# Kernel optimization log

Hardware: AMD Instinct MI355X
Metric: run time of the kernel (lower is better)

The kernel has to match this reference:

```python
import jax, jax.numpy as jnp
import numpy as np

DIM = 512
DIM_TIME = 64
DIM_FF = 2048
B, L = 2, 512
EPS = 1e-5


def _layer_norm(x, g, b):
    mu = jnp.mean(x, axis=-1, keepdims=True)
    var = jnp.mean((x - mu) ** 2, axis=-1, keepdims=True)
    return (x - mu) * jax.lax.rsqrt(var + EPS) * g + b


def _sioconv(u, wa, hid_re, hid_im):
    # u: (B, L, Dt) float. Faithful to the FFT/triu construction, expressed as
    # cumulative log-sums (linear conv with all-ones == causal cumsum).
    Bb, Ll, Dt = u.shape
    out = (u @ wa.T).reshape(Bb, Ll, Dt, 2)          # linear_a, view_as_complex
    a_sqr = out[..., 0] ** 2 + out[..., 1] ** 2
    a = (out[..., 0] + 1j * out[..., 1]) * (jax.lax.rsqrt(a_sqr) * jnp.exp(-a_sqr))
    a = jnp.transpose(a, (0, 2, 1))                  # (B, Dt, L)
    a_ln = jnp.log(a)
    S = jnp.cumsum(a_ln, axis=-1)                    # S_k = sum_{j<=k} ln a_j
    S_prev = jnp.concatenate([jnp.zeros_like(S[..., :1]), S[..., :-1]], axis=-1)
    # c[b,d,i,k] = exp(S_k - S_{i-1}) = prod_{j=i..k} a_j, kept for k >= i-1
    diff = S[:, :, None, :] - S_prev[:, :, :, None]  # (B, Dt, L, L)
    idx = jnp.arange(Ll)
    mask = idx[None, :] >= (idx[:, None] - 1)        # k >= i-1 (triu diag=-1)
    c = jnp.where(mask, jnp.exp(diff), 0.0)
    uc = jnp.transpose(u.astype(jnp.complex64), (0, 2, 1))   # (B, Dt, L)
    hidden = (hid_re + 1j * hid_im)[None, :] * jnp.ones((Bb, 1), jnp.complex64)
    xin = jnp.concatenate([hidden[..., None], uc[..., :-1]], axis=-1)  # rolled + h0
    h = jnp.einsum('bdik,bdk->bdi', c, xin)
    h = h.at[:, :, -1].add(uc[:, :, -1])
    return jnp.transpose(h.real, (0, 2, 1)).astype(u.dtype)


def _ffn(x, w1, b1, w2, b2):
    return jax.nn.silu(x @ w1.T + b1) @ w2.T + b2


def setup_inputs() -> dict:
    key = jax.random.key(0)
    ks = jax.random.split(key, 12)
    d, dt, dff = DIM, DIM_TIME, DIM_FF
    return {
        'x': jax.random.normal(ks[0], (B, L, d), jnp.float32),
        'ln1_g': jnp.ones((d,), jnp.float32), 'ln1_b': jnp.zeros((d,), jnp.float32),
        'fc_w': jax.random.normal(ks[1], (dt, d), jnp.float32) * d ** -0.5,
        'fc_b': jnp.zeros((dt,), jnp.float32),
        'lin_in_w': jax.random.normal(ks[2], (dt, d), jnp.float32) * d ** -0.5,
        'lin_in_b': jnp.zeros((dt,), jnp.float32),
        'wa': jax.random.normal(ks[3], (2 * dt, dt), jnp.float32) * dt ** -0.5,
        'hid_re': jax.random.normal(ks[4], (dt,), jnp.float32),
        'hid_im': jax.random.normal(ks[5], (dt,), jnp.float32),
        'lin_out_w': jax.random.normal(ks[6], (d, dt), jnp.float32) * dt ** -0.5,
        'lin_out_b': jnp.zeros((d,), jnp.float32),
        'ln2_g': jnp.ones((d,), jnp.float32), 'ln2_b': jnp.zeros((d,), jnp.float32),
        'w1': jax.random.normal(ks[7], (dff, d), jnp.float32) * d ** -0.5,
        'b1': jnp.zeros((dff,), jnp.float32),
        'w2': jax.random.normal(ks[8], (d, dff), jnp.float32) * dff ** -0.5,
        'b2': jnp.zeros((d,), jnp.float32),
    }


def reference(x, ln1_g, ln1_b, fc_w, fc_b, lin_in_w, lin_in_b, wa, hid_re, hid_im,
              lin_out_w, lin_out_b, ln2_g, ln2_b, w1, b1, w2, b2):
    x_res = x
    xn = _layer_norm(x, ln1_g, ln1_b)
    y = jax.nn.silu(xn @ fc_w.T + fc_b)                  # gate, (B, L, Dt)
    u = xn @ lin_in_w.T + lin_in_b                       # (B, L, Dt)
    h = _sioconv(u, wa, hid_re, hid_im)
    x = (h * y) @ lin_out_w.T + lin_out_b + x_res        # dropout = identity (eval)
    x_res = x
    x = _ffn(_layer_norm(x, ln2_g, ln2_b), w1, b1, w2, b2) + x_res
    return x
```

## Files before the change

### kernel.cpp

```cpp
#include <hip/hip_runtime.h>
#include <math.h>

#define LSEQ 512
#define DMODEL 512
#define DT 64
#define DFF 2048

typedef unsigned short u16;
typedef __attribute__((ext_vector_type(8))) short short8;
typedef __attribute__((ext_vector_type(4))) float f32x4;

__device__ __forceinline__ float wave_sum(float v) {
#pragma unroll
  for (int o = 32; o > 0; o >>= 1) v += __shfl_xor(v, o, 64);
  return v;
}

__device__ __forceinline__ u16 f2bf(float f) {
  unsigned int u = __float_as_uint(f);
  u += 0x7fffu + ((u >> 16) & 1u);
  return (u16)(u >> 16);
}
__device__ __forceinline__ float bf2f(u16 h) {
  return __uint_as_float(((unsigned int)h) << 16);
}
__device__ __forceinline__ void splitbf(float f, u16& h, u16& l) {
  h = f2bf(f);
  l = f2bf(f - bf2f(h));
}

__device__ __forceinline__ void gload_lds16(const void* g, void* l) {
  __builtin_amdgcn_global_load_lds(
      (const __attribute__((address_space(1))) unsigned int*)g,
      (__attribute__((address_space(3))) unsigned int*)l, 16, 0, 0);
}

__global__ __launch_bounds__(256) void k_cvtall(
    const float* __restrict__ w1, const float* __restrict__ w2,
    const float* __restrict__ fcw, const float* __restrict__ liw,
    const float* __restrict__ wa, const float* __restrict__ low,
    u16* __restrict__ w1b, u16* __restrict__ w2b,
    u16* __restrict__ fclh, u16* __restrict__ fcll,
    u16* __restrict__ wah, u16* __restrict__ wal,
    u16* __restrict__ lowh, u16* __restrict__ lowl)
{
  int i = blockIdx.x * 256 + threadIdx.x;
  if (i >= 550912) return;
  if (i < 524288) {
    const float* s = (i < 262144) ? w1 : w2;
    u16* d = (i < 262144) ? w1b : w2b;
    int off = (i < 262144) ? i : i - 262144;
    float4 v = ((const float4*)s)[off];
    ushort4 o;
    o.x = f2bf(v.x); o.y = f2bf(v.y); o.z = f2bf(v.z); o.w = f2bf(v.w);
    ((ushort4*)d)[off] = o;
    return;
  }
  const float* s; int j; u16 *dh, *dl;
  if (i < 532480)      { s = fcw; j = i - 524288;        dh = fclh; dl = fcll; }
  else if (i < 540672) { s = liw; j = i - 532480 + 8192; dh = fclh; dl = fcll; }
  else if (i < 542720) { s = wa;  j = i - 540672;        dh = wah;  dl = wal;  }
  else                 { s = low; j = i - 542720;        dh = lowh; dl = lowl; }
  int soff = (i < 532480) ? i - 524288 :
             (i < 540672) ? i - 532480 :
             (i < 542720) ? i - 540672 : i - 542720;
  float4 v = ((const float4*)s)[soff];
  ushort4 oh, ol;
  splitbf(v.x, oh.x, ol.x); splitbf(v.y, oh.y, ol.y);
  splitbf(v.z, oh.z, ol.z); splitbf(v.w, oh.w, ol.w);
  ((ushort4*)dh)[j] = oh;
  ((ushort4*)dl)[j] = ol;
}

template<int LO>
__global__ __launch_bounds__(256) void k_ln(
    const float* __restrict__ in, const float* __restrict__ g,
    const float* __restrict__ be, u16* __restrict__ outh, u16* __restrict__ outl)
{
  const int lane = threadIdx.x & 63, wv = threadIdx.x >> 6;
  const int row = blockIdx.x * 4 + wv;
  const float* xr = in + (size_t)row * DMODEL;
  float v[8]; float s = 0.f;
#pragma unroll
  for (int j = 0; j < 8; ++j) { v[j] = xr[lane + 64 * j]; s += v[j]; }
  s = wave_sum(s);
  const float mu = s * (1.f / 512.f);
  float q = 0.f;
#pragma unroll
  for (int j = 0; j < 8; ++j) { float dd = v[j] - mu; q += dd * dd; }
  q = wave_sum(q);
  const float rstd = rsqrtf(q * (1.f / 512.f) + 1e-5f);
#pragma unroll
  for (int j = 0; j < 8; ++j) {
    int idx = lane + 64 * j;
    float o = (v[j] - mu) * rstd * g[idx] + be[idx];
    if constexpr (LO) {
      u16 h, l; splitbf(o, h, l);
      outh[(size_t)row * DMODEL + idx] = h;
      outl[(size_t)row * DMODEL + idx] = l;
    } else {
      outh[(size_t)row * DMODEL + idx] = f2bf(o);
    }
  }
}

__global__ __launch_bounds__(256) void k_proj(
    const u16* __restrict__ xnh, const u16* __restrict__ xnl,
    const u16* __restrict__ fclh, const u16* __restrict__ fcll,
    const float* __restrict__ fcb, const float* __restrict__ lib,
    float* __restrict__ y_o, float* __restrict__ u_o,
    u16* __restrict__ ubh, u16* __restrict__ ubl)
{
  const int w = threadIdx.x >> 6, lane = threadIdx.x & 63;
  const int mt = blockIdx.x, nt = blockIdx.y * 4 + w;
  const int lr = lane & 15, lk = lane >> 4;
  const size_t aoff = (size_t)(mt * 16 + lr) * DMODEL + lk * 8;
  const size_t boff = (size_t)(nt * 16 + lr) * DMODEL + lk * 8;
  f32x4 acc = {};
#pragma unroll 4
  for (int k = 0; k < DMODEL; k += 32) {
    short8 ah = *(const short8*)(xnh + aoff + k);
    short8 al = *(const short8*)(xnl + aoff + k);
    short8 bh = *(const short8*)(fclh + boff + k);
    short8 bl = *(const short8*)(fcll + boff + k);
    acc = __builtin_amdgcn_mfma_f32_16x16x32_bf16(ah, bh, acc, 0, 0, 0);
    acc = __builtin_amdgcn_mfma_f32_16x16x32_bf16(ah, bl, acc, 0, 0, 0);
    acc = __builtin_amdgcn_mfma_f32_16x16x32_bf16(al, bh, acc, 0, 0, 0);
  }
  const int c = nt * 16 + lr;
#pragma unroll
  for (int j = 0; j < 4; ++j) {
    int row = mt * 16 + lk * 4 + j;
    float v = acc[j];
    if (c < DT) {
      v += fcb[c];
      y_o[row * DT + c] = v / (1.f + expf(-v));
    } else {
      int d = c - DT;
      v += lib[d];
      u_o[row * DT + d] = v;
      u16 h, l; splitbf(v, h, l);
      ubh[row * DT + d] = h;
      ubl[row * DT + d] = l;
    }
  }
}

__global__ __launch_bounds__(256) void k_au(
    const u16* __restrict__ ubh, const u16* __restrict__ ubl,
    const u16* __restrict__ wah, const u16* __restrict__ wal,
    float* __restrict__ ar_o, float* __restrict__ ai_o)
{
  const int w = threadIdx.x >> 6, lane = threadIdx.x & 63;
  const int mt = blockIdx.x, nt = blockIdx.y * 4 + w;
  const int lr = lane & 15, lk = lane >> 4;
  const size_t aoff = (size_t)(mt * 16 + lr) * DT + lk * 8;
  const size_t boff = (size_t)(nt * 16 + lr) * DT + lk * 8;
  f32x4 acc = {};
#pragma unroll
  for (int k = 0; k < DT; k += 32) {
    short8 ah = *(const short8*)(ubh + aoff + k);
    short8 al = *(const short8*)(ubl + aoff + k);
    short8 bh = *(const short8*)(wah + boff + k);
    short8 bl = *(const short8*)(wal + boff + k);
    acc = __builtin_amdgcn_mfma_f32_16x16x32_bf16(ah, bh, acc, 0, 0, 0);
    acc = __builtin_amdgcn_mfma_f32_16x16x32_bf16(ah, bl, acc, 0, 0, 0);
    acc = __builtin_amdgcn_mfma_f32_16x16x32_bf16(al, bh, acc, 0, 0, 0);
  }
  const int c = nt * 16 + lr;
#pragma unroll
  for (int j = 0; j < 4; ++j) {
    float v = acc[j];
    float p = __shfl_xor(v, 1, 64);
    float re = (lane & 1) ? p : v;
    float im = (lane & 1) ? v : p;
    float asq = re * re + im * im;
    float sc = rsqrtf(asq) * expf(-asq);
    int row = mt * 16 + lk * 4 + j;
    int d = c >> 1;
    if (lane & 1) ai_o[row * DT + d] = im * sc;
    else          ar_o[row * DT + d] = re * sc;
  }
}

__global__ __launch_bounds__(64) void k_scan2(
    const float* __restrict__ u, const float* __restrict__ ar, const float* __restrict__ ai,
    const float* __restrict__ hr, const float* __restrict__ hi, float* __restrict__ h_o)
{
  const int blk = blockIdx.x;
  const int b = blk >> 6, d = blk & 63;
  const int lane = threadIdx.x;
  const size_t base = (size_t)b * LSEQ * DT + d;
  const int i0 = lane * 8;

  float a_r[8], a_i[8], b_r[8], b_i[8];
#pragma unroll
  for (int e = 0; e < 8; ++e) {
    int i = i0 + e;
    a_r[e] = ar[base + (size_t)i * DT];
    a_i[e] = ai[base + (size_t)i * DT];
    if (i >= 2)      { b_r[e] = u[base + (size_t)(i - 2) * DT]; b_i[e] = 0.f; }
    else if (i == 1) { b_r[e] = hr[d]; b_i[e] = hi[d]; }
    else             { b_r[e] = 0.f;   b_i[e] = 0.f; }
  }

  float Ar = 1.f, Ai = 0.f, Br = 0.f, Bi = 0.f;
#pragma unroll
  for (int e = 0; e < 8; ++e) {
    float nBr = fmaf(Ar, b_r[e], fmaf(-Ai, b_i[e], Br));
    float nBi = fmaf(Ar, b_i[e], fmaf( Ai, b_r[e], Bi));
    float nAr = Ar * a_r[e] - Ai * a_i[e];
    float nAi = Ar * a_i[e] + Ai * a_r[e];
    Ar = nAr; Ai = nAi; Br = nBr; Bi = nBi;
  }

#pragma unroll
  for (int dlt = 1; dlt < 64; dlt <<= 1) {
    float Ar2 = __shfl_down(Ar, dlt, 64);
    float Ai2 = __shfl_down(Ai, dlt, 64);
    float Br2 = __shfl_down(Br, dlt, 64);
    float Bi2 = __shfl_down(Bi, dlt, 64);
    if (lane + dlt < 64) {
      float nAr = Ar * Ar2 - Ai * Ai2;
      float nAi = Ar * Ai2 + Ai * Ar2;
      float nBr = fmaf(Ar, Br2, fmaf(-Ai, Bi2, Br));
      float nBi = fmaf(Ar, Bi2, fmaf( Ai, Br2, Bi));
      Ar = nAr; Ai = nAi; Br = nBr; Bi = nBi;
    }
  }

  float A1r = __shfl_down(Ar, 1, 64), A1i = __shfl_down(Ai, 1, 64);
  float B1r = __shfl_down(Br, 1, 64), B1i = __shfl_down(Bi, 1, 64);
  if (lane == 63) { A1r = 1.f; A1i = 0.f; B1r = 0.f; B1i = 0.f; }
  const float r512 = u[base + (size_t)(LSEQ - 2) * DT];
  float rr = fmaf(A1r, r512, B1r);
  float ri = fmaf(A1i, r512, B1i);

  const float uL = u[base + (size_t)(LSEQ - 1) * DT];
#pragma unroll
  for (int e = 7; e >= 0; --e) {
    int i = i0 + e;
    float nr = fmaf(a_r[e], rr, fmaf(-a_i[e], ri, b_r[e]));
    float ni = fmaf(a_r[e], ri, fmaf( a_i[e], rr, b_i[e]));
    rr = nr; ri = ni;
    float outv = rr;
    if (i == LSEQ - 1) outv += uL;
    h_o[base + (size_t)i * DT] = outv;
  }
}

__global__ __launch_bounds__(256) void k_mid2(
    const float* __restrict__ h, const float* __restrict__ y,
    const u16* __restrict__ lowh, const u16* __restrict__ lowl,
    const float* __restrict__ lob, const float* __restrict__ x,
    float* __restrict__ x2_o)
{
  const int w = threadIdx.x >> 6, lane = threadIdx.x & 63;
  const int mt = blockIdx.x, nt = blockIdx.y * 4 + w;
  const int lr = lane & 15, lk = lane >> 4;
  const int arow = mt * 16 + lr;
  const float* hp = h + (size_t)arow * DT + lk * 8;
  const float* yp = y + (size_t)arow * DT + lk * 8;
  const size_t boff = (size_t)(nt * 16 + lr) * DT + lk * 8;
  f32x4 acc = {};
#pragma unroll
  for (int ks = 0; ks < 2; ++ks) {
    float4 h0 = *(const float4*)(hp + ks * 32);
    float4 h1 = *(const float4*)(hp + ks * 32 + 4);
    float4 y0 = *(const float4*)(yp + ks * 32);
    float4 y1 = *(const float4*)(yp + ks * 32 + 4);
    float pv[8] = {h0.x * y0.x, h0.y * y0.y, h0.z * y0.z, h0.w * y0.w,
                   h1.x * y1.x, h1.y * y1.y, h1.z * y1.z, h1.w * y1.w};
    short8 ah, al;
#pragma unroll
    for (int e = 0; e < 8; ++e) {
      u16 hh, ll; splitbf(pv[e], hh, ll);
      ah[e] = (short)hh; al[e] = (short)ll;
    }
    short8 bh = *(const short8*)(lowh + boff + ks * 32);
    short8 bl = *(const short8*)(lowl + boff + ks * 32);
    acc = __builtin_amdgcn_mfma_f32_16x16x32_bf16(ah, bh, acc, 0, 0, 0);
    acc = __builtin_amdgcn_mfma_f32_16x16x32_bf16(ah, bl, acc, 0, 0, 0);
    acc = __builtin_amdgcn_mfma_f32_16x16x32_bf16(al, bh, acc, 0, 0, 0);
  }
  const int c = nt * 16 + lr;
#pragma unroll
  for (int j = 0; j < 4; ++j) {
    int row = mt * 16 + lk * 4 + j;
    x2_o[(size_t)row * DMODEL + c] = acc[j] + lob[c] + x[(size_t)row * DMODEL + c];
  }
}

template<int BM, int BN, int EPI>
__global__ __launch_bounds__(256) void k_mfma(
    const u16* __restrict__ A, const u16* __restrict__ B,
    const float* __restrict__ bias, float* __restrict__ Cf, u16* __restrict__ Cb,
    int K, int N, int kTiles, int partStride)
{
  constexpr int MF = BM / 32, NF = BN / 32;
  __shared__ __align__(16) u16 As[BM * 64];
  __shared__ __align__(16) u16 Bs[BN * 64];
  const int t = threadIdx.x;
  const int m0 = blockIdx.x * BM, n0 = blockIdx.y * BN;
  const int kBase = blockIdx.z * kTiles * 64;
  const int w = t >> 6, lane = t & 63;
  const int wm = w >> 1, wn = w & 1;
  const int lr = lane & 15, lk = lane >> 4;
  f32x4 acc[MF][NF] = {};

  for (int kt = 0; kt < kTiles; ++kt) {
    const int k0 = kBase + kt * 64;
#pragma unroll
    for (int i = 0; i < BM / 32; ++i) {
      int e = i * 2048 + t * 8;
      int row = e >> 6, col = e & 63;
      gload_lds16(A + (size_t)(m0 + row) * K + k0 + col, &As[e]);
    }
#pragma unroll
    for (int i = 0; i < BN / 32; ++i) {
      int e = i * 2048 + t * 8;
      int row = e >> 6, col = e & 63;
      gload_lds16(B + (size_t)(n0 + row) * K + k0 + col, &Bs[e]);
    }
    __syncthreads();
#pragma unroll
    for (int ks = 0; ks < 2; ++ks) {
      short8 af[MF], bf[NF];
#pragma unroll
      for (int mf = 0; mf < MF; ++mf)
        af[mf] = *(const short8*)&As[(wm * (BM / 2) + mf * 16 + lr) * 64 + ks * 32 + lk * 8];
#pragma unroll
      for (int nf = 0; nf < NF; ++nf)
        bf[nf] = *(const short8*)&Bs[(wn * (BN / 2) + nf * 16 + lr) * 64 + ks * 32 + lk * 8];
#pragma unroll
      for (int mf = 0; mf < MF; ++mf)
#pragma unroll
        for (int nf = 0; nf < NF; ++nf)
          acc[mf][nf] = __builtin_amdgcn_mfma_f32_16x16x32_bf16(af[mf], bf[nf], acc[mf][nf], 0, 0, 0);
    }
    __syncthreads();
  }

#pragma unroll
  for (int mf = 0; mf < MF; ++mf)
#pragma unroll
    for (int nf = 0; nf < NF; ++nf)
#pragma unroll
      for (int j = 0; j < 4; ++j) {
        int rrow = m0 + wm * (BM / 2) + mf * 16 + lk * 4 + j;
        int ccol = n0 + wn * (BN / 2) + nf * 16 + lr;
        if constexpr (EPI == 0) {
          float v = acc[mf][nf][j] + bias[ccol];
          v = v / (1.f + expf(-v));
          Cb[(size_t)rrow * N + ccol] = f2bf(v);
        } else {
          Cf[(size_t)blockIdx.z * partStride + (size_t)rrow * N + ccol] = acc[mf][nf][j];
        }
      }
}

__global__ __launch_bounds__(256) void k_red(
    const float* __restrict__ p, const float* __restrict__ b2,
    const float* __restrict__ x2, float* __restrict__ out, int n4, int partStride4)
{
  int i = blockIdx.x * 256 + threadIdx.x;
  if (i >= n4) return;
  const float4* p4 = (const float4*)p;
  float4 s = p4[i];
  float4 s1 = p4[i + partStride4];
  float4 s2 = p4[i + 2 * partStride4];
  float4 s3 = p4[i + 3 * partStride4];
  s.x += s1.x; s.y += s1.y; s.z += s1.z; s.w += s1.w;
  s.x += s2.x; s.y += s2.y; s.z += s2.z; s.w += s2.w;
  s.x += s3.x; s.y += s3.y; s.z += s3.z; s.w += s3.w;
  int col4 = i & 127;
  float4 bb = ((const float4*)b2)[col4];
  float4 rr = ((const float4*)x2)[i];
  s.x += bb.x + rr.x; s.y += bb.y + rr.y; s.z += bb.z + rr.z; s.w += bb.w + rr.w;
  ((float4*)out)[i] = s;
}

extern "C" void kernel_launch(void* const* d_in, const int* in_sizes, int n_in,
                              void* d_out, int out_size, void* d_ws, size_t ws_size,
                              hipStream_t stream) {
  const float* x    = (const float*)d_in[0];
  const float* ln1g = (const float*)d_in[1];
  const float* ln1b = (const float*)d_in[2];
  const float* fcw  = (const float*)d_in[3];
  const float* fcb  = (const float*)d_in[4];
  const float* liw  = (const float*)d_in[5];
  const float* lib  = (const float*)d_in[6];
  const float* wa   = (const float*)d_in[7];
  const float* hidr = (const float*)d_in[8];
  const float* hidi = (const float*)d_in[9];
  const float* low  = (const float*)d_in[10];
  const float* lob  = (const float*)d_in[11];
  const float* ln2g = (const float*)d_in[12];
  const float* ln2b = (const float*)d_in[13];
  const float* w1   = (const float*)d_in[14];
  const float* b1   = (const float*)d_in[15];
  const float* w2   = (const float*)d_in[16];
  const float* b2   = (const float*)d_in[17];
  float* out = (float*)d_out;
  float* ws  = (float*)d_ws;

  const int R = 2 * LSEQ;
  float* y_    = ws;
  float* u_    = y_   + 65536;
  float* ar_   = u_   + 65536;
  float* ai_   = ar_  + 65536;
  float* h_    = ai_  + 65536;
  float* x2_   = h_   + 65536;
  float* part_ = x2_  + 524288;
  u16* p = (u16*)(part_ + 2097152);
  u16* xnh  = p;            p += 524288;
  u16* xnl  = p;            p += 524288;
  u16* xn2b = p;            p += 524288;
  u16* ubh  = p;            p += 65536;
  u16* ubl  = p;            p += 65536;
  u16* h1b  = p;            p += 2097152;
  u16* w1b  = p;            p += 1048576;
  u16* w2b  = p;            p += 1048576;
  u16* fclh = p;            p += 65536;
  u16* fcll = p;            p += 65536;
  u16* wah  = p;            p += 8192;
  u16* wal  = p;            p += 8192;
  u16* lowh = p;            p += 32768;
  u16* lowl = p;            p += 32768;

  k_cvtall<<<2152, 256, 0, stream>>>(w1, w2, fcw, liw, wa, low,
                                     w1b, w2b, fclh, fcll, wah, wal, lowh, lowl);
  k_ln<1><<<256, 256, 0, stream>>>(x, ln1g, ln1b, xnh, xnl);
  k_proj<<<dim3(64, 2), 256, 0, stream>>>(xnh, xnl, fclh, fcll, fcb, lib,
                                          y_, u_, ubh, ubl);
  k_au<<<dim3(64, 2), 256, 0, stream>>>(ubh, ubl, wah, wal, ar_, ai_);
  k_scan2<<<128, 64, 0, stream>>>(u_, ar_, ai_, hidr, hidi, h_);
  k_mid2<<<dim3(64, 8), 256, 0, stream>>>(h_, y_, lowh, lowl, lob, x, x2_);
  k_ln<0><<<256, 256, 0, stream>>>(x2_, ln2g, ln2b, xn2b, nullptr);
  dim3 g1(R / 64, DFF / 64);
  k_mfma<64, 64, 0><<<g1, 256, 0, stream>>>(xn2b, w1b, b1, nullptr, h1b,
                                            DMODEL, DFF, DMODEL / 64, 0);
  dim3 g2(R / 64, DMODEL / 64, 4);
  k_mfma<64, 64, 2><<<g2, 256, 0, stream>>>(h1b, w2b, nullptr, part_, nullptr,
                                            DFF, DMODEL, (DFF / 4) / 64, R * DMODEL);
  k_red<<<(R * DMODEL / 4 + 255) / 256, 256, 0, stream>>>(part_, b2, x2_, out,
                                                          R * DMODEL / 4, R * DMODEL / 4);
}
```

Baseline: 62.47 us.

## Fuse kernels across pipeline and rewrite FFN GEMMs with 32x32 MFMA

Merges LN1 into the weight-conversion kernel, fuses the projection and linear_a GEMMs into one kernel with the intermediate kept in LDS, and fuses lin_out with LN2. It also replaces the LDS-tiled FFN GEMMs with direct-from-global 32x32x16 MFMA kernels, using an in-block split-K reduction that drops the separate partial-sum reduce kernel. Launch count falls from 10 to 6 and global round trips shrink, but the new FFN kernels read operands without LDS reuse and the fused kernels run with fewer blocks (64).

```diff
diff --git a/kernel.cpp b/kernel.cpp
--- a/kernel.cpp
+++ b/kernel.cpp
@@ -9,6 +9,7 @@
 typedef unsigned short u16;
 typedef __attribute__((ext_vector_type(8))) short short8;
 typedef __attribute__((ext_vector_type(4))) float f32x4;
+typedef __attribute__((ext_vector_type(16))) float f32x16;
 
 __device__ __forceinline__ float wave_sum(float v) {
 #pragma unroll
@@ -29,21 +30,42 @@
   l = f2bf(f - bf2f(h));
 }
 
-__device__ __forceinline__ void gload_lds16(const void* g, void* l) {
-  __builtin_amdgcn_global_load_lds(
-      (const __attribute__((address_space(1))) unsigned int*)g,
-      (__attribute__((address_space(3))) unsigned int*)l, 16, 0, 0);
-}
-
-__global__ __launch_bounds__(256) void k_cvtall(
+__global__ __launch_bounds__(256) void k_pre(
     const float* __restrict__ w1, const float* __restrict__ w2,
     const float* __restrict__ fcw, const float* __restrict__ liw,
     const float* __restrict__ wa, const float* __restrict__ low,
+    const float* __restrict__ x, const float* __restrict__ g1,
+    const float* __restrict__ be1,
     u16* __restrict__ w1b, u16* __restrict__ w2b,
     u16* __restrict__ fclh, u16* __restrict__ fcll,
     u16* __restrict__ wah, u16* __restrict__ wal,
-    u16* __restrict__ lowh, u16* __restrict__ lowl)
-{
+    u16* __restrict__ lowh, u16* __restrict__ lowl,
+    u16* __restrict__ xnh, u16* __restrict__ xnl)
+{
+  if (blockIdx.x >= 2152) {
+    const int lane = threadIdx.x & 63, wv = threadIdx.x >> 6;
+    const int row = (blockIdx.x - 2152) * 4 + wv;
+    const float* xr = x + (size_t)row * DMODEL;
+    float v[8]; float s = 0.f;
+#pragma unroll
+    for (int j = 0; j < 8; ++j) { v[j] = xr[lane + 64 * j]; s += v[j]; }
+    s = wave_sum(s);
+    const float mu = s * (1.f / 512.f);
+    float q = 0.f;
+#pragma unroll
+    for (int j = 0; j < 8; ++j) { float dd = v[j] - mu; q += dd * dd; }
+    q = wave_sum(q);
+    const float rstd = rsqrtf(q * (1.f / 512.f) + 1e-5f);
+#pragma unroll
+    for (int j = 0; j < 8; ++j) {
+      int idx = lane + 64 * j;
+      float o = (v[j] - mu) * rstd * g1[idx] + be1[idx];
+      u16 h, l; splitbf(o, h, l);
+      xnh[(size_t)row * DMODEL + idx] = h;
+      xnl[(size_t)row * DMODEL + idx] = l;
+    }
+    return;
+  }
   int i = blockIdx.x * 256 + threadIdx.x;
   if (i >= 550912) return;
   if (i < 524288) {
@@ -72,114 +94,80 @@
   ((ushort4*)dl)[j] = ol;
 }
 
-template<int LO>
-__global__ __launch_bounds__(256) void k_ln(
-    const float* __restrict__ in, const float* __restrict__ g,
-    const float* __restrict__ be, u16* __restrict__ outh, u16* __restrict__ outl)
-{
-  const int lane = threadIdx.x & 63, wv = threadIdx.x >> 6;
-  const int row = blockIdx.x * 4 + wv;
-  const float* xr = in + (size_t)row * DMODEL;
-  float v[8]; float s = 0.f;
-#pragma unroll
-  for (int j = 0; j < 8; ++j) { v[j] = xr[lane + 64 * j]; s += v[j]; }
-  s = wave_sum(s);
-  const float mu = s * (1.f / 512.f);
-  float q = 0.f;
-#pragma unroll
-  for (int j = 0; j < 8; ++j) { float dd = v[j] - mu; q += dd * dd; }
-  q = wave_sum(q);
-  const float rstd = rsqrtf(q * (1.f / 512.f) + 1e-5f);
-#pragma unroll
-  for (int j = 0; j < 8; ++j) {
-    int idx = lane + 64 * j;
-    float o = (v[j] - mu) * rstd * g[idx] + be[idx];
-    if constexpr (LO) {
-      u16 h, l; splitbf(o, h, l);
-      outh[(size_t)row * DMODEL + idx] = h;
-      outl[(size_t)row * DMODEL + idx] = l;
-    } else {
-      outh[(size_t)row * DMODEL + idx] = f2bf(o);
-    }
-  }
-}
-
-__global__ __launch_bounds__(256) void k_proj(
+__global__ __launch_bounds__(512) void k_fa(
     const u16* __restrict__ xnh, const u16* __restrict__ xnl,
     const u16* __restrict__ fclh, const u16* __restrict__ fcll,
+    const u16* __restrict__ wah, const u16* __restrict__ wal,
     const float* __restrict__ fcb, const float* __restrict__ lib,
     float* __restrict__ y_o, float* __restrict__ u_o,
-    u16* __restrict__ ubh, u16* __restrict__ ubl)
-{
+    float* __restrict__ ar_o, float* __restrict__ ai_o)
+{
+  __shared__ __align__(16) u16 ush[16][80];
+  __shared__ __align__(16) u16 usl[16][80];
   const int w = threadIdx.x >> 6, lane = threadIdx.x & 63;
-  const int mt = blockIdx.x, nt = blockIdx.y * 4 + w;
+  const int mt = blockIdx.x;
   const int lr = lane & 15, lk = lane >> 4;
-  const size_t aoff = (size_t)(mt * 16 + lr) * DMODEL + lk * 8;
-  const size_t boff = (size_t)(nt * 16 + lr) * DMODEL + lk * 8;
-  f32x4 acc = {};
+
+  {
+    const size_t aoff = (size_t)(mt * 16 + lr) * DMODEL + lk * 8;
+    const size_t boff = (size_t)(w * 16 + lr) * DMODEL + lk * 8;
+    f32x4 acc = {};
 #pragma unroll 4
-  for (int k = 0; k < DMODEL; k += 32) {
-    short8 ah = *(const short8*)(xnh + aoff + k);
-    short8 al = *(const short8*)(xnl + aoff + k);
-    short8 bh = *(const short8*)(fclh + boff + k);
-    short8 bl = *(const short8*)(fcll + boff + k);
-    acc = __builtin_amdgcn_mfma_f32_16x16x32_bf16(ah, bh, acc, 0, 0, 0);
-    acc = __builtin_amdgcn_mfma_f32_16x16x32_bf16(ah, bl, acc, 0, 0, 0);
-    acc = __builtin_amdgcn_mfma_f32_16x16x32_bf16(al, bh, acc, 0, 0, 0);
-  }
-  const int c = nt * 16 + lr;
-#pragma unroll
-  for (int j = 0; j < 4; ++j) {
-    int row = mt * 16 + lk * 4 + j;
-    float v = acc[j];
-    if (c < DT) {
-      v += fcb[c];
-      y_o[row * DT + c] = v / (1.f + expf(-v));
-    } else {
-      int d = c - DT;
-      v += lib[d];
-      u_o[row * DT + d] = v;
-      u16 h, l; splitbf(v, h, l);
-      ubh[row * DT + d] = h;
-      ubl[row * DT + d] = l;
-    }
-  }
-}
-
-__global__ __launch_bounds__(256) void k_au(
-    const u16* __restrict__ ubh, const u16* __restrict__ ubl,
-    const u16* __restrict__ wah, const u16* __restrict__ wal,
-    float* __restrict__ ar_o, float* __restrict__ ai_o)
-{
-  const int w = threadIdx.x >> 6, lane = threadIdx.x & 63;
-  const int mt = blockIdx.x, nt = blockIdx.y * 4 + w;
-  const int lr = lane & 15, lk = lane >> 4;
-  const size_t aoff = (size_t)(mt * 16 + lr) * DT + lk * 8;
-  const size_t boff = (size_t)(nt * 16 + lr) * DT + lk * 8;
-  f32x4 acc = {};
-#pragma unroll
-  for (int k = 0; k < DT; k += 32) {
-    short8 ah = *(const short8*)(ubh + aoff + k);
-    short8 al = *(const short8*)(ubl + aoff + k);
-    short8 bh = *(const short8*)(wah + boff + k);
-    short8 bl = *(const short8*)(wal + boff + k);
-    acc = __builtin_amdgcn_mfma_f32_16x16x32_bf16(ah, bh, acc, 0, 0, 0);
-    acc = __builtin_amdgcn_mfma_f32_16x16x32_bf16(ah, bl, acc, 0, 0, 0);
-    acc = __builtin_amdgcn_mfma_f32_16x16x32_bf16(al, bh, acc, 0, 0, 0);
-  }
-  const int c = nt * 16 + lr;
-#pragma unroll
-  for (int j = 0; j < 4; ++j) {
-    float v = acc[j];
-    float p = __shfl_xor(v, 1, 64);
-    float re = (lane & 1) ? p : v;
-    float im = (lane & 1) ? v : p;
-    float asq = re * re + im * im;
-    float sc = rsqrtf(asq) * expf(-asq);
-    int row = mt * 16 + lk * 4 + j;
-    int d = c >> 1;
-    if (lane & 1) ai_o[row * DT + d] = im * sc;
-    else          ar_o[row * DT + d] = re * sc;
+    for (int k = 0; k < DMODEL; k += 32) {
+      short8 ah = *(const short8*)(xnh + aoff + k);
+      short8 al = *(const short8*)(xnl + aoff + k);
+      short8 bh = *(const short8*)(fclh + boff + k);
+      short8 bl = *(const short8*)(fcll + boff + k);
+      acc = __builtin_amdgcn_mfma_f32_16x16x32_bf16(ah, bh, acc, 0, 0, 0);
+      acc = __builtin_amdgcn_mfma_f32_16x16x32_bf16(ah, bl, acc, 0, 0, 0);
+      acc = __builtin_amdgcn_mfma_f32_16x16x32_bf16(al, bh, acc, 0, 0, 0);
+    }
+    const int c = w * 16 + lr;
+#pragma unroll
+    for (int j = 0; j < 4; ++j) {
+      int rl = lk * 4 + j;
+      int row = mt * 16 + rl;
+      float v = acc[j];
+      if (c < DT) {
+        v += fcb[c];
+        y_o[row * DT + c] = v / (1.f + expf(-v));
+      } else {
+        int d = c - DT;
+        v += lib[d];
+        u_o[row * DT + d] = v;
+        u16 h, l; splitbf(v, h, l);
+        ush[rl][d] = h; usl[rl][d] = l;
+      }
+    }
+  }
+  __syncthreads();
+  {
+    const size_t boff = (size_t)(w * 16 + lr) * DT + lk * 8;
+    f32x4 acc = {};
+#pragma unroll
+    for (int ks = 0; ks < 2; ++ks) {
+      short8 ah = *(const short8*)&ush[lr][ks * 32 + lk * 8];
+      short8 al = *(const short8*)&usl[lr][ks * 32 + lk * 8];
+      short8 bh = *(const short8*)(wah + boff + ks * 32);
+      short8 bl = *(const short8*)(wal + boff + ks * 32);
+      acc = __builtin_amdgcn_mfma_f32_16x16x32_bf16(ah, bh, acc, 0, 0, 0);
+      acc = __builtin_amdgcn_mfma_f32_16x16x32_bf16(ah, bl, acc, 0, 0, 0);
+      acc = __builtin_amdgcn_mfma_f32_16x16x32_bf16(al, bh, acc, 0, 0, 0);
+    }
+    const int c = w * 16 + lr;
+#pragma unroll
+    for (int j = 0; j < 4; ++j) {
+      float v = acc[j];
+      float p = __shfl_xor(v, 1, 64);
+      float re = (lane & 1) ? p : v;
+      float im = (lane & 1) ? v : p;
+      float asq = re * re + im * im;
+      float sc = rsqrtf(asq) * expf(-asq);
+      int row = mt * 16 + lk * 4 + j;
+      int d = c >> 1;
+      if (lane & 1) ai_o[row * DT + d] = im * sc;
+      else          ar_o[row * DT + d] = re * sc;
+    }
   }
 }
 
@@ -249,135 +237,131 @@
   }
 }
 
-__global__ __launch_bounds__(256) void k_mid2(
+__global__ __launch_bounds__(512) void k_midln(
     const float* __restrict__ h, const float* __restrict__ y,
     const u16* __restrict__ lowh, const u16* __restrict__ lowl,
     const float* __restrict__ lob, const float* __restrict__ x,
-    float* __restrict__ x2_o)
+    const float* __restrict__ g2, const float* __restrict__ be2,
+    float* __restrict__ x2_o, u16* __restrict__ xn2b)
+{
+  __shared__ __align__(16) u16 hyh[16][80];
+  __shared__ __align__(16) u16 hyl[16][80];
+  __shared__ float x2s[16][520];
+  const int tid = threadIdx.x;
+  const int w = tid >> 6, lane = tid & 63;
+  const int lr = lane & 15, lk = lane >> 4;
+  const int mt = blockIdx.x;
+
+  for (int s = tid; s < 16 * DT; s += 512) {
+    int r = s >> 6, d = s & 63;
+    int row = mt * 16 + r;
+    float v = h[row * DT + d] * y[row * DT + d];
+    u16 hh, ll; splitbf(v, hh, ll);
+    hyh[r][d] = hh; hyl[r][d] = ll;
+  }
+  __syncthreads();
+
+#pragma unroll
+  for (int t = 0; t < 4; ++t) {
+    const int nt = w * 4 + t;
+    const size_t boff = (size_t)(nt * 16 + lr) * DT + lk * 8;
+    f32x4 acc = {};
+#pragma unroll
+    for (int ks = 0; ks < 2; ++ks) {
+      short8 ah = *(const short8*)&hyh[lr][ks * 32 + lk * 8];
+      short8 al = *(const short8*)&hyl[lr][ks * 32 + lk * 8];
+      short8 bh = *(const short8*)(lowh + boff + ks * 32);
+      short8 bl = *(const short8*)(lowl + boff + ks * 32);
+      acc = __builtin_amdgcn_mfma_f32_16x16x32_bf16(ah, bh, acc, 0, 0, 0);
+      acc = __builtin_amdgcn_mfma_f32_16x16x32_bf16(ah, bl, acc, 0, 0, 0);
+      acc = __builtin_amdgcn_mfma_f32_16x16x32_bf16(al, bh, acc, 0, 0, 0);
+    }
+    const int c = nt * 16 + lr;
+#pragma unroll
+    for (int j = 0; j < 4; ++j) {
+      int rl = lk * 4 + j;
+      int row = mt * 16 + rl;
+      float v = acc[j] + lob[c] + x[(size_t)row * DMODEL + c];
+      x2s[rl][c] = v;
+      x2_o[(size_t)row * DMODEL + c] = v;
+    }
+  }
+  __syncthreads();
+
+#pragma unroll
+  for (int rr = 0; rr < 2; ++rr) {
+    const int r = w * 2 + rr;
+    const int row = mt * 16 + r;
+    float v[8]; float s = 0.f;
+#pragma unroll
+    for (int j = 0; j < 8; ++j) { v[j] = x2s[r][lane + 64 * j]; s += v[j]; }
+    s = wave_sum(s);
+    const float mu = s * (1.f / 512.f);
+    float q = 0.f;
+#pragma unroll
+    for (int j = 0; j < 8; ++j) { float dd = v[j] - mu; q += dd * dd; }
+    q = wave_sum(q);
+    const float rstd = rsqrtf(q * (1.f / 512.f) + 1e-5f);
+#pragma unroll
+    for (int j = 0; j < 8; ++j) {
+      int idx = lane + 64 * j;
+      xn2b[(size_t)row * DMODEL + idx] = f2bf((v[j] - mu) * rstd * g2[idx] + be2[idx]);
+    }
+  }
+}
+
+__global__ __launch_bounds__(256) void k_ffn1(
+    const u16* __restrict__ A, const u16* __restrict__ B,
+    const float* __restrict__ bias, u16* __restrict__ C)
 {
   const int w = threadIdx.x >> 6, lane = threadIdx.x & 63;
   const int mt = blockIdx.x, nt = blockIdx.y * 4 + w;
-  const int lr = lane & 15, lk = lane >> 4;
-  const int arow = mt * 16 + lr;
-  const float* hp = h + (size_t)arow * DT + lk * 8;
-  const float* yp = y + (size_t)arow * DT + lk * 8;
-  const size_t boff = (size_t)(nt * 16 + lr) * DT + lk * 8;
-  f32x4 acc = {};
-#pragma unroll
-  for (int ks = 0; ks < 2; ++ks) {
-    float4 h0 = *(const float4*)(hp + ks * 32);
-    float4 h1 = *(const float4*)(hp + ks * 32 + 4);
-    float4 y0 = *(const float4*)(yp + ks * 32);
-    float4 y1 = *(const float4*)(yp + ks * 32 + 4);
-    float pv[8] = {h0.x * y0.x, h0.y * y0.y, h0.z * y0.z, h0.w * y0.w,
-                   h1.x * y1.x, h1.y * y1.y, h1.z * y1.z, h1.w * y1.w};
-    short8 ah, al;
-#pragma unroll
-    for (int e = 0; e < 8; ++e) {
-      u16 hh, ll; splitbf(pv[e], hh, ll);
-      ah[e] = (short)hh; al[e] = (short)ll;
-    }
-    short8 bh = *(const short8*)(lowh + boff + ks * 32);
-    short8 bl = *(const short8*)(lowl + boff + ks * 32);
-    acc = __builtin_amdgcn_mfma_f32_16x16x32_bf16(ah, bh, acc, 0, 0, 0);
-    acc = __builtin_amdgcn_mfma_f32_16x16x32_bf16(ah, bl, acc, 0, 0, 0);
-    acc = __builtin_amdgcn_mfma_f32_16x16x32_bf16(al, bh, acc, 0, 0, 0);
-  }
-  const int c = nt * 16 + lr;
-#pragma unroll
-  for (int j = 0; j < 4; ++j) {
-    int row = mt * 16 + lk * 4 + j;
-    x2_o[(size_t)row * DMODEL + c] = acc[j] + lob[c] + x[(size_t)row * DMODEL + c];
-  }
-}
-
-template<int BM, int BN, int EPI>
-__global__ __launch_bounds__(256) void k_mfma(
+  const int l32 = lane & 31, hi = lane >> 5;
+  const u16* a = A + (size_t)(mt * 32 + l32) * DMODEL + hi * 8;
+  const u16* b = B + (size_t)(nt * 32 + l32) * DMODEL + hi * 8;
+  f32x16 acc = {};
+#pragma unroll 8
+  for (int k = 0; k < DMODEL; k += 16)
+    acc = __builtin_amdgcn_mfma_f32_32x32x16_bf16(*(const short8*)(a + k),
+                                                  *(const short8*)(b + k), acc, 0, 0, 0);
+  const int col = nt * 32 + l32;
+  const float bb = bias[col];
+#pragma unroll
+  for (int r = 0; r < 16; ++r) {
+    int row = mt * 32 + (r & 3) + 8 * (r >> 2) + 4 * hi;
+    float v = acc[r] + bb;
+    v = v / (1.f + expf(-v));
+    C[(size_t)row * DFF + col] = f2bf(v);
+  }
+}
+
+__global__ __launch_bounds__(256) void k_ffn2(
     const u16* __restrict__ A, const u16* __restrict__ B,
-    const float* __restrict__ bias, float* __restrict__ Cf, u16* __restrict__ Cb,
-    int K, int N, int kTiles, int partStride)
-{
-  constexpr int MF = BM / 32, NF = BN / 32;
-  __shared__ __align__(16) u16 As[BM * 64];
-  __shared__ __align__(16) u16 Bs[BN * 64];
-  const int t = threadIdx.x;
-  const int m0 = blockIdx.x * BM, n0 = blockIdx.y * BN;
-  const int kBase = blockIdx.z * kTiles * 64;
-  const int w = t >> 6, lane = t & 63;
-  const int wm = w >> 1, wn = w & 1;
-  const int lr = lane & 15, lk = lane >> 4;
-  f32x4 acc[MF][NF] = {};
-
-  for (int kt = 0; kt < kTiles; ++kt) {
-    const int k0 = kBase + kt * 64;
-#pragma unroll
-    for (int i = 0; i < BM / 32; ++i) {
-      int e = i * 2048 + t * 8;
-      int row = e >> 6, col = e & 63;
-      gload_lds16(A + (size_t)(m0 + row) * K + k0 + col, &As[e]);
-    }
-#pragma unroll
-    for (int i = 0; i < BN / 32; ++i) {
-      int e = i * 2048 + t * 8;
-      int row = e >> 6, col = e & 63;
-      gload_lds16(B + (size_t)(n0 + row) * K + k0 + col, &Bs[e]);
-    }
-    __syncthreads();
-#pragma unroll
-    for (int ks = 0; ks < 2; ++ks) {
-      short8 af[MF], bf[NF];
-#pragma unroll
-      for (int mf = 0; mf < MF; ++mf)
-        af[mf] = *(const short8*)&As[(wm * (BM / 2) + mf * 16 + lr) * 64 + ks * 32 + lk * 8];
-#pragma unroll
-      for (int nf = 0; nf < NF; ++nf)
-        bf[nf] = *(const short8*)&Bs[(wn * (BN / 2) + nf * 16 + lr) * 64 + ks * 32 + lk * 8];
-#pragma unroll
-      for (int mf = 0; mf < MF; ++mf)
-#pragma unroll
-        for (int nf = 0; nf < NF; ++nf)
-          acc[mf][nf] = __builtin_amdgcn_mfma_f32_16x16x32_bf16(af[mf], bf[nf], acc[mf][nf], 0, 0, 0);
-    }
-    __syncthreads();
-  }
-
-#pragma unroll
-  for (int mf = 0; mf < MF; ++mf)
-#pragma unroll
-    for (int nf = 0; nf < NF; ++nf)
-#pragma unroll
-      for (int j = 0; j < 4; ++j) {
-        int rrow = m0 + wm * (BM / 2) + mf * 16 + lk * 4 + j;
-        int ccol = n0 + wn * (BN / 2) + nf * 16 + lr;
-        if constexpr (EPI == 0) {
-          float v = acc[mf][nf][j] + bias[ccol];
-          v = v / (1.f + expf(-v));
-          Cb[(size_t)rrow * N + ccol] = f2bf(v);
-        } else {
-          Cf[(size_t)blockIdx.z * partStride + (size_t)rrow * N + ccol] = acc[mf][nf][j];
-        }
-      }
-}
-
-__global__ __launch_bounds__(256) void k_red(
-    const float* __restrict__ p, const float* __restrict__ b2,
-    const float* __restrict__ x2, float* __restrict__ out, int n4, int partStride4)
-{
-  int i = blockIdx.x * 256 + threadIdx.x;
-  if (i >= n4) return;
-  const float4* p4 = (const float4*)p;
-  float4 s = p4[i];
-  float4 s1 = p4[i + partStride4];
-  float4 s2 = p4[i + 2 * partStride4];
-  float4 s3 = p4[i + 3 * partStride4];
-  s.x += s1.x; s.y += s1.y; s.z += s1.z; s.w += s1.w;
-  s.x += s2.x; s.y += s2.y; s.z += s2.z; s.w += s2.w;
-  s.x += s3.x; s.y += s3.y; s.z += s3.z; s.w += s3.w;
-  int col4 = i & 127;
-  float4 bb = ((const float4*)b2)[col4];
-  float4 rr = ((const float4*)x2)[i];
-  s.x += bb.x + rr.x; s.y += bb.y + rr.y; s.z += bb.z + rr.z; s.w += bb.w + rr.w;
-  ((float4*)out)[i] = s;
+    const float* __restrict__ b2, const float* __restrict__ x2,
+    float* __restrict__ out)
+{
+  __shared__ float red[4][16][64];
+  const int w = threadIdx.x >> 6, lane = threadIdx.x & 63;
+  const int mt = blockIdx.x, nt = blockIdx.y;
+  const int l32 = lane & 31, hi = lane >> 5;
+  const u16* a = A + (size_t)(mt * 32 + l32) * DFF + w * 512 + hi * 8;
+  const u16* b = B + (size_t)(nt * 32 + l32) * DFF + w * 512 + hi * 8;
+  f32x16 acc = {};
+#pragma unroll 8
+  for (int k = 0; k < 512; k += 16)
+    acc = __builtin_amdgcn_mfma_f32_32x32x16_bf16(*(const short8*)(a + k),
+                                                  *(const short8*)(b + k), acc, 0, 0, 0);
+#pragma unroll
+  for (int r = 0; r < 16; ++r) red[w][r][lane] = acc[r];
+  __syncthreads();
+  for (int s = threadIdx.x; s < 1024; s += 256) {
+    int r = s >> 6, l = s & 63;
+    float v = red[0][r][l] + red[1][r][l] + red[2][r][l] + red[3][r][l];
+    int row = mt * 32 + (r & 3) + 8 * (r >> 2) + 4 * (l >> 5);
+    int col = nt * 32 + (l & 31);
+    out[(size_t)row * DMODEL + col] =
+        v + b2[col] + x2[(size_t)row * DMODEL + col];
+  }
 }
 
 extern "C" void kernel_launch(void* const* d_in, const int* in_sizes, int n_in,
@@ -404,20 +388,16 @@
   float* out = (float*)d_out;
   float* ws  = (float*)d_ws;
 
-  const int R = 2 * LSEQ;
-  float* y_    = ws;
-  float* u_    = y_   + 65536;
-  float* ar_   = u_   + 65536;
-  float* ai_   = ar_  + 65536;
-  float* h_    = ai_  + 65536;
-  float* x2_   = h_   + 65536;
-  float* part_ = x2_  + 524288;
-  u16* p = (u16*)(part_ + 2097152);
+  float* y_   = ws;
+  float* u_   = y_  + 65536;
+  float* ar_  = u_  + 65536;
+  float* ai_  = ar_ + 65536;
+  float* h_   = ai_ + 65536;
+  float* x2_  = h_  + 65536;
+  u16* p = (u16*)(x2_ + 524288);
   u16* xnh  = p;            p += 524288;
   u16* xnl  = p;            p += 524288;
   u16* xn2b = p;            p += 524288;
-  u16* ubh  = p;            p += 65536;
-  u16* ubl  = p;            p += 65536;
   u16* h1b  = p;            p += 2097152;
   u16* w1b  = p;            p += 1048576;
   u16* w2b  = p;            p += 1048576;
@@ -428,21 +408,14 @@
   u16* lowh = p;            p += 32768;
   u16* lowl = p;            p += 32768;
 
-  k_cvtall<<<2152, 256, 0, stream>>>(w1, w2, fcw, liw, wa, low,
-                                     w1b, w2b, fclh, fcll, wah, wal, lowh, lowl);
-  k_ln<1><<<256, 256, 0, stream>>>(x, ln1g, ln1b, xnh, xnl);
-  k_proj<<<dim3(64, 2), 256, 0, stream>>>(xnh, xnl, fclh, fcll, fcb, lib,
-                                          y_, u_, ubh, ubl);
-  k_au<<<dim3(64, 2), 256, 0, stream>>>(ubh, ubl, wah, wal, ar_, ai_);
+  k_pre<<<2408, 256, 0, stream>>>(w1, w2, fcw, liw, wa, low, x, ln1g, ln1b,
+                                  w1b, w2b, fclh, fcll, wah, wal, lowh, lowl,
+                                  xnh, xnl);
+  k_fa<<<64, 512, 0, stream>>>(xnh, xnl, fclh, fcll, wah, wal, fcb, lib,
+                               y_, u_, ar_, ai_);
   k_scan2<<<128, 64, 0, stream>>>(u_, ar_, ai_, hidr, hidi, h_);
-  k_mid2<<<dim3(64, 8), 256, 0, stream>>>(h_, y_, lowh, lowl, lob, x, x2_);
-  k_ln<0><<<256, 256, 0, stream>>>(x2_, ln2g, ln2b, xn2b, nullptr);
-  dim3 g1(R / 64, DFF / 64);
-  k_mfma<64, 64, 0><<<g1, 256, 0, stream>>>(xn2b, w1b, b1, nullptr, h1b,
-                                            DMODEL, DFF, DMODEL / 64, 0);
-  dim3 g2(R / 64, DMODEL / 64, 4);
-  k_mfma<64, 64, 2><<<g2, 256, 0, stream>>>(h1b, w2b, nullptr, part_, nullptr,
-                                            DFF, DMODEL, (DFF / 4) / 64, R * DMODEL);
-  k_red<<<(R * DMODEL / 4 + 255) / 256, 256, 0, stream>>>(part_, b2, x2_, out,
-                                                          R * DMODEL / 4, R * DMODEL / 4);
-}
+  k_midln<<<64, 512, 0, stream>>>(h_, y_, lowh, lowl, lob, x, ln2g, ln2b,
+                                  x2_, xn2b);
+  k_ffn1<<<dim3(32, 16), 256, 0, stream>>>(xn2b, w1b, b1, h1b);
+  k_ffn2<<<dim3(32, 16), 256, 0, stream>>>(h1b, w2b, b2, x2_, out);
+}
```

Measured after the change: 80.31 us. 28.6% more time.
